# Optimization experiments

Measured on AMD Instinct MI355X. Metric: run time of the kernel, lower is better.

## Reference

```python
import jax, jax.numpy as jnp
import numpy as np

B, T, C = 2, 2048, 2048
NH, NKV = 16, 4
HD = C // NH  # 128


def setup_inputs() -> dict:
    key = jax.random.key(0)
    ks = jax.random.split(key, 5)
    w = lambda k, shape: jax.random.normal(k, shape, jnp.float32) * 0.02
    return {
        "x": jax.random.normal(ks[0], (B, T, C), jnp.float32),
        "Wq": w(ks[1], (C, C)),
        "Wk": w(ks[2], (C, NKV * HD)),
        "Wv": w(ks[3], (C, NKV * HD)),
        "Wproj": w(ks[4], (C, C)),
    }


def _rope(x):
    # x: [B, H, T, D]; rotate-half RoPE with base 10000
    D = x.shape[-1]
    t = x.shape[-2]
    inv_freq = 1.0 / (10000.0 ** (jnp.arange(0, D, 2, dtype=jnp.float32) / D))
    freqs = jnp.arange(t, dtype=jnp.float32)[:, None] * inv_freq[None, :]  # [T, D/2]
    emb = jnp.concatenate([freqs, freqs], axis=-1)  # [T, D]
    cos, sin = jnp.cos(emb), jnp.sin(emb)
    x1, x2 = x[..., : D // 2], x[..., D // 2 :]
    rotated = jnp.concatenate([-x2, x1], axis=-1)
    return x * cos + rotated * sin


def reference(x, Wq, Wk, Wv, Wproj):
    b, t, c = x.shape
    q = (x @ Wq).reshape(b, t, NH, HD).transpose(0, 2, 1, 3)    # [B,NH,T,HD]
    k = (x @ Wk).reshape(b, t, NKV, HD).transpose(0, 2, 1, 3)   # [B,NKV,T,HD]
    v = (x @ Wv).reshape(b, t, NKV, HD).transpose(0, 2, 1, 3)
    q = _rope(q)
    k = _rope(k)
    rep = NH // NKV
    k = jnp.repeat(k, rep, axis=1)  # [B,NH,T,HD]
    v = jnp.repeat(v, rep, axis=1)
    scale = 1.0 / jnp.sqrt(jnp.float32(HD))
    scores = jnp.einsum("bhqd,bhkd->bhqk", q, k) * scale        # [B,NH,T,T]
    causal = jnp.tril(jnp.ones((t, t), dtype=bool))
    scores = jnp.where(causal, scores, jnp.finfo(scores.dtype).min)
    attn = jax.nn.softmax(scores, axis=-1)
    y = jnp.einsum("bhqk,bhkd->bhqd", attn, v)                  # [B,NH,T,HD]
    y = y.transpose(0, 2, 1, 3).reshape(b, t, c)
    return y @ Wproj
```

## Files before the change

kernel.cpp:

```cpp
#include <hip/hip_runtime.h>

#define B_ 2
#define T_ 2048
#define C_ 2048
#define NH_ 16
#define NKV_ 4
#define HD_ 128
#define M_ 4096
#define NQKV_ 3072

typedef __bf16 bf16x8 __attribute__((ext_vector_type(8)));
typedef float f32x4 __attribute__((ext_vector_type(4)));
typedef float f32x16 __attribute__((ext_vector_type(16)));

__device__ __forceinline__ unsigned short f2bf(float f) {
  union { float f; unsigned u; } c{f};
  unsigned u = c.u + 0x7FFFu + ((c.u >> 16) & 1u);
  return (unsigned short)(u >> 16);
}
__device__ __forceinline__ float bf2f(unsigned short h) {
  union { unsigned u; float f; } c{(unsigned)h << 16};
  return c.f;
}

#define GLOAD_LDS16(g, l)                                        \
  __builtin_amdgcn_global_load_lds(                              \
      (const __attribute__((address_space(1))) void*)(g),        \
      (__attribute__((address_space(3))) void*)(l), 16, 0, 0)

__global__ void rope_table_kernel(float2* __restrict__ rt) {
  int t = blockIdx.x, i = threadIdx.x;
  float inv = powf(10000.f, -(float)(2 * i) / 128.f);
  float s, c;
  sincosf((float)t * inv, &s, &c);
  rt[t * 64 + i] = make_float2(c, s);
}

__global__ void convx_kernel(const float* __restrict__ x, unsigned short* __restrict__ xb, int n4) {
  int i = blockIdx.x * blockDim.x + threadIdx.x;
  if (i >= n4) return;
  float4 v = reinterpret_cast<const float4*>(x)[i];
  union { ushort4 u; unsigned short s[4]; } o;
  o.s[0] = f2bf(v.x); o.s[1] = f2bf(v.y); o.s[2] = f2bf(v.z); o.s[3] = f2bf(v.w);
  reinterpret_cast<ushort4*>(xb)[i] = o.u;
}

__global__ void transpose_conv_kernel(const float* __restrict__ W, unsigned short* __restrict__ Wt,
                                      int K, int N) {
  __shared__ float tile[32][33];
  int bx = blockIdx.x * 32;
  int by = blockIdx.y * 32;
  int tx = threadIdx.x & 31, ty = threadIdx.x >> 5;
#pragma unroll
  for (int r = 0; r < 32; r += 8)
    tile[ty + r][tx] = W[(size_t)(by + ty + r) * N + bx + tx];
  __syncthreads();
#pragma unroll
  for (int r = 0; r < 32; r += 8)
    Wt[(size_t)(bx + ty + r) * K + by + tx] = f2bf(tile[tx][ty + r]);
}

__global__ void rope_kernel(unsigned short* __restrict__ qkv, const float2* __restrict__ rt) {
  int g = blockIdx.x * blockDim.x + threadIdx.x;
  if (g >= M_ * 160) return;
  int m = g / 160, u = g - m * 160;
  int t = m & (T_ - 1);
  int io, col0;
  if (u < 128) { io = (u & 7) * 8; col0 = (u >> 3) * HD_ + io; }
  else         { int uu = u - 128; io = (uu & 7) * 8; col0 = C_ + (uu >> 3) * HD_ + io; }
  unsigned short* p = qkv + (size_t)m * NQKV_ + col0;
  union V8 { uint4 v; unsigned short s[8]; };
  V8 a, b, oa, ob;
  a.v = *reinterpret_cast<const uint4*>(p);
  b.v = *reinterpret_cast<const uint4*>(p + 64);
#pragma unroll
  for (int j = 0; j < 8; ++j) {
    float2 cs = rt[t * 64 + io + j];
    float x1 = bf2f(a.s[j]), x2 = bf2f(b.s[j]);
    oa.s[j] = f2bf(x1 * cs.x - x2 * cs.y);
    ob.s[j] = f2bf(x2 * cs.x + x1 * cs.y);
  }
  *reinterpret_cast<uint4*>(p) = oa.v;
  *reinterpret_cast<uint4*>(p + 64) = ob.v;
}

__global__ void transpose_v_kernel(const unsigned short* __restrict__ qkv,
                                   unsigned short* __restrict__ vt) {
  __shared__ unsigned short tile[32][33];
  int bh = blockIdx.z;
  int b = bh >> 2, kvh = bh & 3;
  int t0 = blockIdx.x * 32, d0 = blockIdx.y * 32;
  int tx = threadIdx.x & 31, ty = threadIdx.x >> 5;
#pragma unroll
  for (int r = 0; r < 32; r += 8)
    tile[ty + r][tx] = qkv[(size_t)(b * T_ + t0 + ty + r) * NQKV_ + 2560 + kvh * HD_ + d0 + tx];
  __syncthreads();
#pragma unroll
  for (int r = 0; r < 32; r += 8)
    vt[(size_t)(bh * HD_ + d0 + ty + r) * T_ + t0 + tx] = tile[tx][ty + r];
}

template <typename OUT>
__global__ __launch_bounds__(256) void gemm_bf16(const unsigned short* __restrict__ A,
                                                 const unsigned short* __restrict__ Bt,
                                                 OUT* __restrict__ Cm,
                                                 int M, int N, int K) {
  constexpr int BK = 32;
  __shared__ __align__(16) unsigned short Al[2][128 * BK];
  __shared__ __align__(16) unsigned short Bl[2][128 * BK];
  int tid = threadIdx.x, w = tid >> 6, lane = tid & 63;
  int l15 = lane & 15, l4 = lane >> 4;
  int wr = w >> 1, wc = w & 1;
  size_t arow0 = (size_t)blockIdx.y * 128;
  size_t brow0 = (size_t)blockIdx.x * 128;

  f32x4 acc[4][4];
#pragma unroll
  for (int mi = 0; mi < 4; ++mi)
#pragma unroll
    for (int ni = 0; ni < 4; ++ni) acc[mi][ni] = (f32x4){0.f, 0.f, 0.f, 0.f};

  auto stage = [&](int buf, int k0) {
#pragma unroll
    for (int i = 0; i < 2; ++i) {
      int c = i * 256 + w * 64 + lane;
      const unsigned short* g = A + (arow0 + (c >> 2)) * K + k0 + (c & 3) * 8;
      GLOAD_LDS16(g, &Al[buf][(i * 4 + w) * 512]);
    }
#pragma unroll
    for (int i = 0; i < 2; ++i) {
      int c = i * 256 + w * 64 + lane;
      const unsigned short* g = Bt + (brow0 + (c >> 2)) * K + k0 + (c & 3) * 8;
      GLOAD_LDS16(g, &Bl[buf][(i * 4 + w) * 512]);
    }
  };

  stage(0, 0);
  __syncthreads();
  int NT = K / BK, cur = 0;
  for (int kt = 0; kt < NT; ++kt) {
    if (kt + 1 < NT) stage(cur ^ 1, (kt + 1) * BK);
    const unsigned short* Ab = &Al[cur][0];
    const unsigned short* Bb = &Bl[cur][0];
    bf16x8 af[4], bfr[4];
#pragma unroll
    for (int mi = 0; mi < 4; ++mi)
      af[mi] = *reinterpret_cast<const bf16x8*>(Ab + (wr * 64 + mi * 16 + l15) * BK + l4 * 8);
#pragma unroll
    for (int ni = 0; ni < 4; ++ni)
      bfr[ni] = *reinterpret_cast<const bf16x8*>(Bb + (wc * 64 + ni * 16 + l15) * BK + l4 * 8);
#pragma unroll
    for (int mi = 0; mi < 4; ++mi)
#pragma unroll
      for (int ni = 0; ni < 4; ++ni)
        acc[mi][ni] = __builtin_amdgcn_mfma_f32_16x16x32_bf16(af[mi], bfr[ni], acc[mi][ni], 0, 0, 0);
    __syncthreads();
    cur ^= 1;
  }

#pragma unroll
  for (int mi = 0; mi < 4; ++mi)
#pragma unroll
    for (int ni = 0; ni < 4; ++ni) {
      size_t row = arow0 + wr * 64 + mi * 16 + l4 * 4;
      size_t col = brow0 + wc * 64 + ni * 16 + l15;
#pragma unroll
      for (int r = 0; r < 4; ++r) {
        float v = acc[mi][ni][r];
        if constexpr (sizeof(OUT) == 4) Cm[(row + r) * N + col] = v;
        else                            Cm[(row + r) * N + col] = f2bf(v);
      }
    }
}

__global__ __launch_bounds__(256, 2) void attn_kernel(const unsigned short* __restrict__ qkv,
                                                      const unsigned short* __restrict__ vt,
                                                      unsigned short* __restrict__ att) {
  constexpr int KB = 64;
  __shared__ __align__(16) unsigned short Kl[2][KB * 128];
  __shared__ __align__(16) unsigned short Vl[2][128 * KB];
  int tid = threadIdx.x, w = tid >> 6, lane = tid & 63;
  int l31 = lane & 31, hi = lane >> 5;
  int h4 = hi * 4;

  int id = blockIdx.x;
  int u = id & 255, half = id >> 8;
  int bh = u & 31;
  int qh = u >> 5;
  int qi = half ? (15 - qh) : qh;
  int q0 = qi * 128;
  int b = bh >> 4, hd = bh & 15, kvh = hd >> 2;
  int qr0 = q0 + w * 32;
  int ql = qr0 + l31;

  bf16x8 qf[8];
  {
    const unsigned short* qb = qkv + (size_t)(b * T_ + ql) * NQKV_ + hd * HD_ + hi * 8;
    const float scale = 0.08838834764831845f;
#pragma unroll
    for (int df = 0; df < 8; ++df) {
      bf16x8 t = *reinterpret_cast<const bf16x8*>(qb + df * 16);
#pragma unroll
      for (int j = 0; j < 8; ++j) t[j] = (__bf16)((float)t[j] * scale);
      qf[df] = t;
    }
  }

  f32x16 o[4];
#pragma unroll
  for (int dt = 0; dt < 4; ++dt)
#pragma unroll
    for (int r = 0; r < 16; ++r) o[dt][r] = 0.f;
  float mr = -1e30f, lr = 0.f;

  auto stage = [&](int buf, int kv0) {
#pragma unroll
    for (int i = 0; i < 4; ++i) {
      int c = (i * 4 + w) * 64 + lane;
      int g = c ^ ((c >> 4) & 7);
      const unsigned short* src =
          qkv + (size_t)(b * T_ + kv0 + (g >> 4)) * NQKV_ + C_ + kvh * HD_ + (g & 15) * 8;
      GLOAD_LDS16(src, &Kl[buf][(i * 4 + w) * 512]);
    }
#pragma unroll
    for (int i = 0; i < 4; ++i) {
      int c = (i * 4 + w) * 64 + lane;
      int g = c ^ ((c >> 3) & 7);
      const unsigned short* src =
          vt + (size_t)((b * NKV_ + kvh) * HD_ + (g >> 3)) * T_ + kv0 + (g & 7) * 8;
      GLOAD_LDS16(src, &Vl[buf][(i * 4 + w) * 512]);
    }
  };

  int nt = q0 / KB + 2;
  stage(0, 0);
  __syncthreads();
  int cur = 0;
  for (int kt = 0; kt < nt; ++kt) {
    int kv0 = kt * KB;
    if (kt + 1 < nt) stage(cur ^ 1, kv0 + KB);

    if (kv0 <= qr0 + 31) {
      f32x16 s[2];
#pragma unroll
      for (int r = 0; r < 16; ++r) { s[0][r] = 0.f; s[1][r] = 0.f; }
      __builtin_amdgcn_s_setprio(1);
#pragma unroll
      for (int t2 = 0; t2 < 2; ++t2)
#pragma unroll
        for (int df = 0; df < 8; ++df) {
          bf16x8 kf = *reinterpret_cast<const bf16x8*>(
              &Kl[cur][((t2 * 32 + l31) * 128 + df * 16 + hi * 8) ^ ((l31 & 7) << 3)]);
          s[t2] = __builtin_amdgcn_mfma_f32_32x32x16_bf16(kf, qf[df], s[t2], 0, 0, 0);
        }
      __builtin_amdgcn_s_setprio(0);

      bool need_mask = (kv0 + KB - 1) > qr0;
      float rm = -1e30f;
#pragma unroll
      for (int t2 = 0; t2 < 2; ++t2)
#pragma unroll
        for (int r = 0; r < 16; ++r) {
          float sv = s[t2][r];
          int kcol = kv0 + t2 * 32 + (r & 3) + 8 * (r >> 2) + h4;
          if (need_mask && kcol > ql) sv = -1e30f;
          s[t2][r] = sv;
          rm = fmaxf(rm, sv);
        }
      rm = fmaxf(rm, __shfl_xor(rm, 32));

      if (!__all(rm <= mr + 8.f)) {
        float mnew = fmaxf(mr, rm);
        float alpha = __expf(mr - mnew);
        mr = mnew;
        lr *= alpha;
#pragma unroll
        for (int dt = 0; dt < 4; ++dt)
#pragma unroll
          for (int r = 0; r < 16; ++r) o[dt][r] *= alpha;
      }

      float ps = 0.f;
#pragma unroll
      for (int t2 = 0; t2 < 2; ++t2)
#pragma unroll
        for (int r = 0; r < 16; ++r) {
          float p = __expf(s[t2][r] - mr);
          s[t2][r] = p;
          ps += p;
        }
      lr += ps;

      unsigned pk[2][8];
#pragma unroll
      for (int t2 = 0; t2 < 2; ++t2)
#pragma unroll
        for (int i = 0; i < 8; ++i) {
          union { unsigned u32; __bf16 hh[2]; } pr;
          pr.hh[0] = (__bf16)s[t2][2 * i];
          pr.hh[1] = (__bf16)s[t2][2 * i + 1];
          pk[t2][i] = pr.u32;
        }

      bf16x8 pb[4];
#pragma unroll
      for (int f = 0; f < 4; ++f) {
        int t2 = f >> 1, bq = (f & 1) * 4;
        union { bf16x8 v; unsigned d[4]; } fr;
#pragma unroll
        for (int p = 0; p < 2; ++p) {
          unsigned uu = pk[t2][bq + p];
          unsigned ww = pk[t2][bq + 2 + p];
          unsigned us = (unsigned)__shfl_xor((int)uu, 32);
          unsigned ws = (unsigned)__shfl_xor((int)ww, 32);
          fr.d[p]     = hi ? ws : uu;
          fr.d[2 + p] = hi ? ww : us;
        }
        pb[f] = fr.v;
      }

      __builtin_amdgcn_s_setprio(1);
#pragma unroll
      for (int dt = 0; dt < 4; ++dt)
#pragma unroll
        for (int kf = 0; kf < 4; ++kf) {
          bf16x8 vf = *reinterpret_cast<const bf16x8*>(
              &Vl[cur][((dt * 32 + l31) * KB + kf * 16 + hi * 8) ^ ((l31 & 7) << 3)]);
          o[dt] = __builtin_amdgcn_mfma_f32_32x32x16_bf16(vf, pb[kf], o[dt], 0, 0, 0);
        }
      __builtin_amdgcn_s_setprio(0);
    }

    __syncthreads();
    cur ^= 1;
  }

  float ls = lr + __shfl_xor(lr, 32);
  float inv = 1.f / ls;
  unsigned short* ob = att + (size_t)(b * T_ + ql) * C_ + hd * HD_;
#pragma unroll
  for (int dt = 0; dt < 4; ++dt)
#pragma unroll
    for (int r = 0; r < 16; ++r) {
      int d = dt * 32 + (r & 3) + 8 * (r >> 2) + h4;
      ob[d] = f2bf(o[dt][r] * inv);
    }
}

extern "C" void kernel_launch(void* const* d_in, const int* in_sizes, int n_in,
                              void* d_out, int out_size, void* d_ws, size_t ws_size,
                              hipStream_t stream) {
  const float* x  = (const float*)d_in[0];
  const float* Wq = (const float*)d_in[1];
  const float* Wk = (const float*)d_in[2];
  const float* Wv = (const float*)d_in[3];
  const float* Wp = (const float*)d_in[4];
  float* out = (float*)d_out;
  char* ws = (char*)d_ws;

  unsigned short* xb  = (unsigned short*)(ws);
  unsigned short* wt  = (unsigned short*)(ws + 16777216);
  unsigned short* qkv = (unsigned short*)(ws + 37748736);
  float2*         rt  = (float2*)(ws + 62914560);
  unsigned short* vt  = (unsigned short*)(ws + 63963136);
  unsigned short* att = xb;

  rope_table_kernel<<<T_, 64, 0, stream>>>(rt);
  convx_kernel<<<(M_ * C_ / 4 + 255) / 256, 256, 0, stream>>>(x, xb, M_ * C_ / 4);
  transpose_conv_kernel<<<dim3(64, 64), 256, 0, stream>>>(Wq, wt, C_, C_);
  transpose_conv_kernel<<<dim3(16, 64), 256, 0, stream>>>(Wk, wt + (size_t)2048 * 2048, C_, 512);
  transpose_conv_kernel<<<dim3(16, 64), 256, 0, stream>>>(Wv, wt + (size_t)2560 * 2048, C_, 512);
  transpose_conv_kernel<<<dim3(64, 64), 256, 0, stream>>>(Wp, wt + (size_t)3072 * 2048, C_, 2048);

  gemm_bf16<unsigned short><<<dim3(NQKV_ / 128, M_ / 128), 256, 0, stream>>>(
      xb, wt, qkv, M_, NQKV_, C_);
  rope_kernel<<<(M_ * 160 + 255) / 256, 256, 0, stream>>>(qkv, rt);
  transpose_v_kernel<<<dim3(T_ / 32, HD_ / 32, B_ * NKV_), 256, 0, stream>>>(qkv, vt);
  attn_kernel<<<dim3(512), 256, 0, stream>>>(qkv, vt, att);
  gemm_bf16<float><<<dim3(C_ / 128, M_ / 128), 256, 0, stream>>>(
      att, wt + (size_t)3072 * 2048, out, M_, C_, C_);
}
```

Baseline: 234.0 us.

## Split K/V staging into separate pipelined buffers and merge weight transposes

```diff
diff --git a/kernel.cpp b/kernel.cpp
--- a/kernel.cpp
+++ b/kernel.cpp
@@ -45,11 +45,20 @@
   reinterpret_cast<ushort4*>(xb)[i] = o.u;
 }
 
-__global__ void transpose_conv_kernel(const float* __restrict__ W, unsigned short* __restrict__ Wt,
-                                      int K, int N) {
+__global__ void transpose_conv4_kernel(const float* __restrict__ Wq, const float* __restrict__ Wk,
+                                       const float* __restrict__ Wv, const float* __restrict__ Wp,
+                                       unsigned short* __restrict__ wt) {
   __shared__ float tile[32][33];
-  int bx = blockIdx.x * 32;
-  int by = blockIdx.y * 32;
+  int id = blockIdx.x;
+  const float* W;
+  unsigned short* Wt;
+  int N, bx, by;
+  if (id < 4096)      { W = Wq; Wt = wt;                          N = 2048; int u = id;        bx = u & 63; by = u >> 6; }
+  else if (id < 5120) { W = Wk; Wt = wt + (size_t)2048 * 2048;    N = 512;  int u = id - 4096; bx = u & 15; by = u >> 4; }
+  else if (id < 6144) { W = Wv; Wt = wt + (size_t)2560 * 2048;    N = 512;  int u = id - 5120; bx = u & 15; by = u >> 4; }
+  else                { W = Wp; Wt = wt + (size_t)3072 * 2048;    N = 2048; int u = id - 6144; bx = u & 63; by = u >> 6; }
+  const int K = 2048;
+  bx *= 32; by *= 32;
   int tx = threadIdx.x & 31, ty = threadIdx.x >> 5;
 #pragma unroll
   for (int r = 0; r < 32; r += 8)
@@ -177,7 +186,7 @@
                                                       const unsigned short* __restrict__ vt,
                                                       unsigned short* __restrict__ att) {
   constexpr int KB = 64;
-  __shared__ __align__(16) unsigned short Kl[2][KB * 128];
+  __shared__ __align__(16) unsigned short Kl[3][KB * 128];
   __shared__ __align__(16) unsigned short Vl[2][128 * KB];
   int tid = threadIdx.x, w = tid >> 6, lane = tid & 63;
   int l31 = lane & 31, hi = lane >> 5;
@@ -213,7 +222,10 @@
     for (int r = 0; r < 16; ++r) o[dt][r] = 0.f;
   float mr = -1e30f, lr = 0.f;
 
-  auto stage = [&](int buf, int kv0) {
+  int nt = q0 / KB + 2;
+
+  auto stage_K = [&](int buf, int tile) {
+    int kv0 = tile * KB;
 #pragma unroll
     for (int i = 0; i < 4; ++i) {
       int c = (i * 4 + w) * 64 + lane;
@@ -222,6 +234,9 @@
           qkv + (size_t)(b * T_ + kv0 + (g >> 4)) * NQKV_ + C_ + kvh * HD_ + (g & 15) * 8;
       GLOAD_LDS16(src, &Kl[buf][(i * 4 + w) * 512]);
     }
+  };
+  auto stage_V = [&](int buf, int tile) {
+    int kv0 = tile * KB;
 #pragma unroll
     for (int i = 0; i < 4; ++i) {
       int c = (i * 4 + w) * 64 + lane;
@@ -232,25 +247,35 @@
     }
   };
 
-  int nt = q0 / KB + 2;
-  stage(0, 0);
-  __syncthreads();
-  int cur = 0;
+  stage_K(0, 0);
+  stage_V(0, 0);
+  stage_K(1, nt > 1 ? 1 : 0);
+
   for (int kt = 0; kt < nt; ++kt) {
     int kv0 = kt * KB;
-    if (kt + 1 < nt) stage(cur ^ 1, kv0 + KB);
-
-    if (kv0 <= qr0 + 31) {
-      f32x16 s[2];
+    int tv = kt + 1 < nt ? kt + 1 : nt - 1;
+    int tk = kt + 2 < nt ? kt + 2 : nt - 1;
+    stage_V((kt + 1) & 1, tv);
+    stage_K((kt + 2) % 3, tk);
+
+    asm volatile("s_waitcnt vmcnt(16)" ::: "memory");
+    __builtin_amdgcn_s_barrier();
+    asm volatile("" ::: "memory");
+
+    bool active = (kv0 <= qr0 + 31);
+    f32x16 s[2];
+    unsigned pk[2][8];
+    if (active) {
 #pragma unroll
       for (int r = 0; r < 16; ++r) { s[0][r] = 0.f; s[1][r] = 0.f; }
+      const unsigned short* Kb = &Kl[kt % 3][0];
       __builtin_amdgcn_s_setprio(1);
 #pragma unroll
       for (int t2 = 0; t2 < 2; ++t2)
 #pragma unroll
         for (int df = 0; df < 8; ++df) {
           bf16x8 kf = *reinterpret_cast<const bf16x8*>(
-              &Kl[cur][((t2 * 32 + l31) * 128 + df * 16 + hi * 8) ^ ((l31 & 7) << 3)]);
+              Kb + (((t2 * 32 + l31) * 128 + df * 16 + hi * 8) ^ ((l31 & 7) << 3)));
           s[t2] = __builtin_amdgcn_mfma_f32_32x32x16_bf16(kf, qf[df], s[t2], 0, 0, 0);
         }
       __builtin_amdgcn_s_setprio(0);
@@ -291,7 +316,6 @@
         }
       lr += ps;
 
-      unsigned pk[2][8];
 #pragma unroll
       for (int t2 = 0; t2 < 2; ++t2)
 #pragma unroll
@@ -301,7 +325,13 @@
           pr.hh[1] = (__bf16)s[t2][2 * i + 1];
           pk[t2][i] = pr.u32;
         }
-
+    }
+
+    asm volatile("s_waitcnt vmcnt(12)" ::: "memory");
+    __builtin_amdgcn_s_barrier();
+    asm volatile("" ::: "memory");
+
+    if (active) {
       bf16x8 pb[4];
 #pragma unroll
       for (int f = 0; f < 4; ++f) {
@@ -319,20 +349,21 @@
         pb[f] = fr.v;
       }
 
+      const unsigned short* Vb = &Vl[kt & 1][0];
       __builtin_amdgcn_s_setprio(1);
 #pragma unroll
       for (int dt = 0; dt < 4; ++dt)
 #pragma unroll
         for (int kf = 0; kf < 4; ++kf) {
           bf16x8 vf = *reinterpret_cast<const bf16x8*>(
-              &Vl[cur][((dt * 32 + l31) * KB + kf * 16 + hi * 8) ^ ((l31 & 7) << 3)]);
+              Vb + (((dt * 32 + l31) * KB + kf * 16 + hi * 8) ^ ((l31 & 7) << 3)));
           o[dt] = __builtin_amdgcn_mfma_f32_32x32x16_bf16(vf, pb[kf], o[dt], 0, 0, 0);
         }
       __builtin_amdgcn_s_setprio(0);
     }
 
-    __syncthreads();
-    cur ^= 1;
+    __builtin_amdgcn_s_barrier();
+    asm volatile("" ::: "memory");
   }
 
   float ls = lr + __shfl_xor(lr, 32);
@@ -367,10 +398,7 @@
 
   rope_table_kernel<<<T_, 64, 0, stream>>>(rt);
   convx_kernel<<<(M_ * C_ / 4 + 255) / 256, 256, 0, stream>>>(x, xb, M_ * C_ / 4);
-  transpose_conv_kernel<<<dim3(64, 64), 256, 0, stream>>>(Wq, wt, C_, C_);
-  transpose_conv_kernel<<<dim3(16, 64), 256, 0, stream>>>(Wk, wt + (size_t)2048 * 2048, C_, 512);
-  transpose_conv_kernel<<<dim3(16, 64), 256, 0, stream>>>(Wv, wt + (size_t)2560 * 2048, C_, 512);
-  transpose_conv_kernel<<<dim3(64, 64), 256, 0, stream>>>(Wp, wt + (size_t)3072 * 2048, C_, 2048);
+  transpose_conv4_kernel<<<dim3(10240), 256, 0, stream>>>(Wq, Wk, Wv, Wp, wt);
 
   gemm_bf16<unsigned short><<<dim3(NQKV_ / 128, M_ / 128), 256, 0, stream>>>(
       xb, wt, qkv, M_, NQKV_, C_);
```

Result: no change. 234.5 us (+0.2%).
